# Kernel tuning notes

Hardware: AMD Instinct MI355X
Metric: run time of the kernel (lower is better)

## Reference

```python
import jax, jax.numpy as jnp
import numpy as np
from jax import lax

L, D, S, T, BATCH, NC = 4, 256, 64, 2048, 64, 10
EPS = 1e-5


def setup_inputs() -> dict:
    key = jax.random.key(0)
    ks = iter(jax.random.split(key, 16))
    n = lambda shape, s=1.0: jax.random.normal(next(ks), shape, dtype=jnp.float32) * s
    return {
        "x": n((BATCH, 1, T)),
        "emb_w": n((D, 1), 0.1), "emb_b": jnp.zeros((D,), jnp.float32),
        "Am": n((L, S, S), 0.01), "Bm": n((L, S, D), 0.01),
        "Cm": n((L, D, S), 0.01), "Dm": n((L, D, D), 0.01),
        "in_w": n((L, D, D), 0.05), "in_b": jnp.zeros((L, D), jnp.float32),
        "out_w": n((L, D, D), 0.05), "out_b": jnp.zeros((L, D), jnp.float32),
        "s4ln_w": jnp.ones((L, D), jnp.float32), "s4ln_b": jnp.zeros((L, D), jnp.float32),
        "ln_w": jnp.ones((L, D), jnp.float32), "ln_b": jnp.zeros((L, D), jnp.float32),
        "c1_w": n((512, D), 0.05), "c1_b": jnp.zeros((512,), jnp.float32),
        "bn1_g": jnp.ones((512,), jnp.float32), "bn1_b": jnp.zeros((512,), jnp.float32),
        "bn1_m": jnp.zeros((512,), jnp.float32), "bn1_v": jnp.ones((512,), jnp.float32),
        "c2_w": n((256, 512), 0.05), "c2_b": jnp.zeros((256,), jnp.float32),
        "bn2_g": jnp.ones((256,), jnp.float32), "bn2_b": jnp.zeros((256,), jnp.float32),
        "bn2_m": jnp.zeros((256,), jnp.float32), "bn2_v": jnp.ones((256,), jnp.float32),
        "c3_w": n((NC, 256), 0.05), "c3_b": jnp.zeros((NC,), jnp.float32),
    }


def _ln(x, w, b):
    m = jnp.mean(x, axis=-1, keepdims=True)
    v = jnp.mean((x - m) ** 2, axis=-1, keepdims=True)
    return (x - m) * lax.rsqrt(v + EPS) * w + b


def reference(x, emb_w, emb_b, Am, Bm, Cm, Dm, in_w, in_b, out_w, out_b,
              s4ln_w, s4ln_b, ln_w, ln_b, c1_w, c1_b, bn1_g, bn1_b, bn1_m, bn1_v,
              c2_w, c2_b, bn2_g, bn2_b, bn2_m, bn2_v, c3_w, c3_b):
    # x: (B, 1, T) -> (B, T, 1) -> embed to (B, T, D)
    h = jnp.transpose(x, (0, 2, 1)) @ emb_w.T + emb_b
    Bsz = h.shape[0]
    for l in range(L):
        res = h
        u = _ln(h @ in_w[l].T + in_b[l], s4ln_w[l], s4ln_b[l])  # input_proj + norm
        # precompute time-invariant input drives: (T, B, S) and (T, B, D)
        uB = jnp.einsum('btd,sd->tbs', u, Bm[l])
        uD = jnp.einsum('btd,ed->tbe', u, Dm[l])
        A = Am[l]

        def step(s, ub):  # s_t = s_{t-1} @ A^T + x_t @ B^T
            s = s @ A.T + ub
            return s, s

        _, hs = lax.scan(step, jnp.zeros((Bsz, S), h.dtype), uB)  # hs: (T, B, S)
        y = jnp.einsum('tbs,ds->btd', hs, Cm[l]) + jnp.transpose(uD, (1, 0, 2))
        y = y @ out_w[l].T + out_b[l]  # output_proj (dropout = identity in eval)
        h = _ln(y + res, ln_w[l], ln_b[l])  # residual + outer LayerNorm
    pooled = jnp.mean(h, axis=1)  # AdaptiveAvgPool1d(1) over time -> (B, D)
    z = pooled @ c1_w.T + c1_b
    z = jax.nn.relu((z - bn1_m) * lax.rsqrt(bn1_v + EPS) * bn1_g + bn1_b)
    z = z @ c2_w.T + c2_b
    z = jax.nn.relu((z - bn2_m) * lax.rsqrt(bn2_v + EPS) * bn2_g + bn2_b)
    return z @ c3_w.T + c3_b
```

## Files before the change

kernel.cpp:

```cpp
#include <hip/hip_runtime.h>


#define EPSF 1e-5f

typedef _Float16 F16;
typedef _Float16 half8 __attribute__((ext_vector_type(8)));
typedef float f32x4 __attribute__((ext_vector_type(4)));

constexpr int  Bc  = 64;
constexpr int  Tc  = 2048;
constexpr int  Dc  = 256;
constexpr int  Sc  = 64;
constexpr int  Lc  = 4;
constexpr int  KC  = 12;
constexpr int  NCc = 10;
constexpr int  PAD = 16;
constexpr long BT  = (long)Bc * Tc;
constexpr int  TPB = Tc + PAD;

constexpr size_t OFF_H16  = 0;
constexpr size_t OFF_U16  = OFF_H16 + (size_t)BT * Dc * 2;
constexpr size_t OFF_UBP  = OFF_U16 + (size_t)BT * Dc * 2;
constexpr size_t OFF_S16  = OFF_UBP + (size_t)Bc * TPB * Sc * 2;
constexpr size_t OFF_T16  = OFF_S16 + (size_t)BT * Sc * 2;
constexpr size_t OFF_IW16 = OFF_T16 + (size_t)Lc * KC * Sc * Sc * 2;
constexpr size_t OFF_OW16 = OFF_IW16 + (size_t)Lc * Dc * Dc * 2;
constexpr size_t OFF_BM16 = OFF_OW16 + (size_t)Lc * Dc * Dc * 2;
constexpr size_t OFF_CM16 = OFF_BM16 + (size_t)Lc * Sc * Dc * 2;
constexpr size_t OFF_DM16 = OFF_CM16 + (size_t)Lc * Dc * Sc * 2;
constexpr size_t OFF_PP   = OFF_DM16 + (size_t)Lc * Dc * Dc * 2;
constexpr size_t WS_NEED  = OFF_PP + (size_t)Bc * 32 * Dc * 4;

#define MFMA16(a, b, c) __builtin_amdgcn_mfma_f32_16x16x32_f16((a), (b), (c), 0, 0, 0)

__global__ __launch_bounds__(256) void diag_kernel(float* __restrict__ outp,
                                                   int n, float wsmb)
{
    int i = blockIdx.x * 256 + threadIdx.x;
    if (i < n) outp[i] = (i == 0) ? wsmb : 0.f;
}

__global__ __launch_bounds__(256) void cvt16_kernel(
    const float* __restrict__ src, F16* __restrict__ dst)
{
    long i = ((long)blockIdx.x * 256 + threadIdx.x) * 8;
    float4 a = *(const float4*)(src + i);
    float4 b = *(const float4*)(src + i + 4);
    half8 h;
    h[0] = (F16)a.x; h[1] = (F16)a.y; h[2] = (F16)a.z; h[3] = (F16)a.w;
    h[4] = (F16)b.x; h[5] = (F16)b.y; h[6] = (F16)b.z; h[7] = (F16)b.w;
    *(half8*)(dst + i) = h;
}

__global__ __launch_bounds__(256) void embed_kernel(
    const float* __restrict__ x, const float* __restrict__ ew,
    const float* __restrict__ eb, F16* __restrict__ h16)
{
    long i = ((long)blockIdx.x * 256 + threadIdx.x) * 8;
    int d = (int)(i & 255);
    long bt = i >> 8;
    float xv = x[bt];
    float4 w0 = *(const float4*)(ew + d), w1 = *(const float4*)(ew + d + 4);
    float4 b0 = *(const float4*)(eb + d), b1 = *(const float4*)(eb + d + 4);
    half8 h;
    h[0] = (F16)fmaf(xv, w0.x, b0.x); h[1] = (F16)fmaf(xv, w0.y, b0.y);
    h[2] = (F16)fmaf(xv, w0.z, b0.z); h[3] = (F16)fmaf(xv, w0.w, b0.w);
    h[4] = (F16)fmaf(xv, w1.x, b1.x); h[5] = (F16)fmaf(xv, w1.y, b1.y);
    h[6] = (F16)fmaf(xv, w1.z, b1.z); h[7] = (F16)fmaf(xv, w1.w, b1.w);
    *(half8*)(h16 + i) = h;
}

__global__ __launch_bounds__(256) void apow_kernel(
    const float* __restrict__ Am, F16* __restrict__ taps)
{
    int l = blockIdx.x;
    const float* A = Am + (long)l * Sc * Sc;
    F16* out = taps + (long)l * KC * Sc * Sc;
    __shared__ float sA[64][68];
    __shared__ float sP[64][68];
    int tid = threadIdx.x;

    for (int idx = tid; idx < 64 * 16; idx += 256) {
        int r = idx >> 4, q = idx & 15;
        float4 v = *(const float4*)(A + r * 64 + q * 4);
        *(float4*)&sA[r][q * 4] = v;
        float4 id;
        id.x = (q * 4 + 0 == r) ? 1.f : 0.f;
        id.y = (q * 4 + 1 == r) ? 1.f : 0.f;
        id.z = (q * 4 + 2 == r) ? 1.f : 0.f;
        id.w = (q * 4 + 3 == r) ? 1.f : 0.f;
        *(float4*)&sP[r][q * 4] = id;
        out[r * 64 + q * 4 + 0] = (F16)id.x;
        out[r * 64 + q * 4 + 1] = (F16)id.y;
        out[r * 64 + q * 4 + 2] = (F16)id.z;
        out[r * 64 + q * 4 + 3] = (F16)id.w;
    }
    __syncthreads();

    int rb = (tid >> 4) * 4;
    int cb = (tid & 15) * 4;
    for (int k = 1; k < KC; ++k) {
        float nacc[4][4];
#pragma unroll
        for (int i = 0; i < 4; i++)
#pragma unroll
            for (int u = 0; u < 4; u++) nacc[i][u] = 0.f;
        for (int s = 0; s < 64; ++s) {
            float4 p = *(const float4*)&sP[s][cb];
#pragma unroll
            for (int i = 0; i < 4; i++) {
                float a = sA[rb + i][s];
                nacc[i][0] = fmaf(a, p.x, nacc[i][0]);
                nacc[i][1] = fmaf(a, p.y, nacc[i][1]);
                nacc[i][2] = fmaf(a, p.z, nacc[i][2]);
                nacc[i][3] = fmaf(a, p.w, nacc[i][3]);
            }
        }
        __syncthreads();
#pragma unroll
        for (int i = 0; i < 4; i++) {
            *(float4*)&sP[rb + i][cb] = make_float4(nacc[i][0], nacc[i][1], nacc[i][2], nacc[i][3]);
#pragma unroll
            for (int c = 0; c < 4; c++)
                out[(long)k * 4096 + (rb + i) * 64 + cb + c] = (F16)nacc[i][c];
        }
        __syncthreads();
    }
}

__global__ __launch_bounds__(256) void zeropad_kernel(F16* __restrict__ ubp)
{
    long i8 = ((long)blockIdx.x * 256 + threadIdx.x) * 8;
    int b = (int)(i8 >> 10);
    int off = (int)(i8 & 1023);
    *(uint4*)(ubp + (long)b * TPB * Sc + off) = make_uint4(0u, 0u, 0u, 0u);
}

template<int DIR>
__global__ __launch_bounds__(512) void mfma_gemm_ln_kernel(
    const F16* X, F16* out, const F16* __restrict__ W,
    const float* __restrict__ bias,
    const float* __restrict__ lnw, const float* __restrict__ lnb)
{
    __shared__ half8 sW[16 * 8 * 64];
    const int tid = threadIdx.x;
    const int lane = tid & 63, wv = tid >> 6;
    const int r15 = lane & 15, hi4 = lane >> 4;

#pragma unroll
    for (int it = 0; it < 16; ++it) {
        int fid = tid + it * 512;
        int l2 = fid & 63, pair = fid >> 6;
        int n = pair >> 3, ks = pair & 7;
        sW[fid] = *(const half8*)(W + (n * 16 + (l2 & 15)) * Dc + ks * 32 + (l2 >> 4) * 8);
    }
    __syncthreads();

    const long m0 = (long)blockIdx.x * 256 + wv * 32;

    f32x4 acc[2][16];
#pragma unroll
    for (int r2 = 0; r2 < 2; ++r2)
#pragma unroll
        for (int n = 0; n < 16; ++n) acc[r2][n] = f32x4{0.f, 0.f, 0.f, 0.f};

    const F16* xb = X + (m0 + r15) * Dc + (hi4 << 3);

    for (int ks = 0; ks < 8; ++ks) {
        half8 a0 = *(const half8*)(xb + ks * 32);
        half8 a1 = *(const half8*)(xb + 16 * Dc + ks * 32);
#pragma unroll
        for (int n = 0; n < 16; ++n) {
            half8 b = sW[(n * 8 + ks) * 64 + lane];
            acc[0][n] = MFMA16(a0, b, acc[0][n]);
            acc[1][n] = MFMA16(a1, b, acc[1][n]);
        }
    }

    float bv[16], gw[16], gb[16];
#pragma unroll
    for (int n = 0; n < 16; ++n) {
        int c = n * 16 + r15;
        bv[n] = bias[c]; gw[n] = lnw[c]; gb[n] = lnb[c];
    }

#pragma unroll
    for (int r2 = 0; r2 < 2; ++r2) {
        const long rowb = m0 + r2 * 16 + hi4 * 4;
        float sum[4] = {0.f, 0.f, 0.f, 0.f}, ssq[4] = {0.f, 0.f, 0.f, 0.f};
#pragma unroll
        for (int n = 0; n < 16; ++n)
#pragma unroll
            for (int r = 0; r < 4; ++r) {
                float v = acc[r2][n][r] + bv[n];
                if (DIR) v += (float)out[(rowb + r) * Dc + n * 16 + r15];
                acc[r2][n][r] = v;
                sum[r] += v;
                ssq[r] = fmaf(v, v, ssq[r]);
            }
#pragma unroll
        for (int r = 0; r < 4; ++r) {
#pragma unroll
            for (int m = 1; m < 16; m <<= 1) {
                sum[r] += __shfl_xor(sum[r], m);
                ssq[r] += __shfl_xor(ssq[r], m);
            }
            float mean = sum[r] * (1.f / 256.f);
            float var  = fmaf(-mean, mean, ssq[r] * (1.f / 256.f));
            sum[r] = mean;
            ssq[r] = rsqrtf(var + EPSF);
        }
#pragma unroll
        for (int n = 0; n < 16; ++n)
#pragma unroll
            for (int r = 0; r < 4; ++r) {
                float val = fmaf((acc[r2][n][r] - sum[r]) * ssq[r], gw[n], gb[n]);
                out[(rowb + r) * Dc + n * 16 + r15] = (F16)val;
            }
    }
}

__global__ __launch_bounds__(512) void mfma_ub_kernel(
    const F16* __restrict__ X, const F16* __restrict__ W, F16* __restrict__ UBP)
{
    __shared__ half8 sW[4 * 8 * 64];
    const int tid = threadIdx.x;
    const int lane = tid & 63, wv = tid >> 6;
    const int r15 = lane & 15, hi4 = lane >> 4;

#pragma unroll
    for (int it = 0; it < 4; ++it) {
        int fid = tid + it * 512;
        int l2 = fid & 63, pair = fid >> 6;
        int n = pair >> 3, ks = pair & 7;
        sW[fid] = *(const half8*)(W + (n * 16 + (l2 & 15)) * Dc + ks * 32 + (l2 >> 4) * 8);
    }
    __syncthreads();

    const long m0 = (long)blockIdx.x * 256 + wv * 32;
    const long b  = m0 >> 11;
    const long tl = m0 & (Tc - 1);

    f32x4 acc[2][4];
#pragma unroll
    for (int r2 = 0; r2 < 2; ++r2)
#pragma unroll
        for (int n = 0; n < 4; ++n) acc[r2][n] = f32x4{0.f, 0.f, 0.f, 0.f};

    const F16* xb = X + (m0 + r15) * Dc + (hi4 << 3);

    for (int ks = 0; ks < 8; ++ks) {
        half8 a0 = *(const half8*)(xb + ks * 32);
        half8 a1 = *(const half8*)(xb + 16 * Dc + ks * 32);
#pragma unroll
        for (int n = 0; n < 4; ++n) {
            half8 bfr = sW[(n * 8 + ks) * 64 + lane];
            acc[0][n] = MFMA16(a0, bfr, acc[0][n]);
            acc[1][n] = MFMA16(a1, bfr, acc[1][n]);
        }
    }

#pragma unroll
    for (int r2 = 0; r2 < 2; ++r2) {
        const long rowb = b * TPB + PAD + tl + r2 * 16 + hi4 * 4;
#pragma unroll
        for (int n = 0; n < 4; ++n)
#pragma unroll
            for (int r = 0; r < 4; ++r)
                UBP[(rowb + r) * Sc + n * 16 + r15] = (F16)acc[r2][n][r];
    }
}

__global__ __launch_bounds__(512) void mfma_conv_kernel(
    const F16* __restrict__ UBP, const F16* __restrict__ T16, F16* __restrict__ S16)
{
    __shared__ half8 sT[12 * 4 * 2 * 64];
    const int tid = threadIdx.x;
    const int lane = tid & 63, wv = tid >> 6;
    const int r15 = lane & 15, hi4 = lane >> 4;

#pragma unroll
    for (int it = 0; it < 12; ++it) {
        int fid = tid + it * 512;
        int l2 = fid & 63, rest = fid >> 6;
        int k = rest >> 3, nk = rest & 7;
        int n = nk >> 1, ks = nk & 1;
        sT[fid] = *(const half8*)(T16 + (long)k * 4096 +
                                  (n * 16 + (l2 & 15)) * Sc + ks * 32 + (l2 >> 4) * 8);
    }
    __syncthreads();

    const long m0 = (long)blockIdx.x * 256 + wv * 32;
    const long b  = m0 >> 11;
    const long tl = m0 & (Tc - 1);

    f32x4 acc[2][4];
#pragma unroll
    for (int r2 = 0; r2 < 2; ++r2)
#pragma unroll
        for (int n = 0; n < 4; ++n) acc[r2][n] = f32x4{0.f, 0.f, 0.f, 0.f};

    const long abase = (b * TPB + PAD + tl + r15) * Sc + (hi4 << 3);

    for (int k = 0; k < KC; ++k) {
        const F16* ap = UBP + abase - (long)k * Sc;
#pragma unroll
        for (int ks = 0; ks < 2; ++ks) {
            half8 a0 = *(const half8*)(ap + ks * 32);
            half8 a1 = *(const half8*)(ap + 16 * Sc + ks * 32);
#pragma unroll
            for (int n = 0; n < 4; ++n) {
                half8 bfr = sT[(k * 8 + n * 2 + ks) * 64 + lane];
                acc[0][n] = MFMA16(a0, bfr, acc[0][n]);
                acc[1][n] = MFMA16(a1, bfr, acc[1][n]);
            }
        }
    }

#pragma unroll
    for (int r2 = 0; r2 < 2; ++r2) {
        const long rowb = m0 + r2 * 16 + hi4 * 4;
#pragma unroll
        for (int n = 0; n < 4; ++n)
#pragma unroll
            for (int r = 0; r < 4; ++r)
                S16[(rowb + r) * Sc + n * 16 + r15] = (F16)acc[r2][n][r];
    }
}

__global__ __launch_bounds__(512) void mfma_k4_kernel(
    const F16* __restrict__ S16, const F16* __restrict__ C16,
    const F16* U16, const F16* __restrict__ D16, F16* Y16)
{
    __shared__ half8 sD[16 * 8 * 64];
    const int tid = threadIdx.x;
    const int lane = tid & 63, wv = tid >> 6;
    const int r15 = lane & 15, hi4 = lane >> 4;

#pragma unroll
    for (int it = 0; it < 16; ++it) {
        int fid = tid + it * 512;
        int l2 = fid & 63, pair = fid >> 6;
        int n = pair >> 3, ks = pair & 7;
        sD[fid] = *(const half8*)(D16 + (n * 16 + (l2 & 15)) * Dc + ks * 32 + (l2 >> 4) * 8);
    }
    __syncthreads();

    const long m0 = (long)blockIdx.x * 256 + wv * 32;

    f32x4 acc[2][16];
#pragma unroll
    for (int r2 = 0; r2 < 2; ++r2)
#pragma unroll
        for (int n = 0; n < 16; ++n) acc[r2][n] = f32x4{0.f, 0.f, 0.f, 0.f};

    const F16* sb = S16 + (m0 + r15) * Sc + (hi4 << 3);
    const F16* cw = C16 + (long)r15 * Sc + (hi4 << 3);
#pragma unroll
    for (int ks = 0; ks < 2; ++ks) {
        half8 a0 = *(const half8*)(sb + ks * 32);
        half8 a1 = *(const half8*)(sb + 16 * Sc + ks * 32);
#pragma unroll
        for (int n = 0; n < 16; ++n) {
            half8 bfr = *(const half8*)(cw + n * 16 * Sc + ks * 32);
            acc[0][n] = MFMA16(a0, bfr, acc[0][n]);
            acc[1][n] = MFMA16(a1, bfr, acc[1][n]);
        }
    }

    const F16* ub = U16 + (m0 + r15) * Dc + (hi4 << 3);
    for (int ks = 0; ks < 8; ++ks) {
        half8 a0 = *(const half8*)(ub + ks * 32);
        half8 a1 = *(const half8*)(ub + 16 * Dc + ks * 32);
#pragma unroll
        for (int n = 0; n < 16; ++n) {
            half8 bfr = sD[(n * 8 + ks) * 64 + lane];
            acc[0][n] = MFMA16(a0, bfr, acc[0][n]);
            acc[1][n] = MFMA16(a1, bfr, acc[1][n]);
        }
    }

#pragma unroll
    for (int r2 = 0; r2 < 2; ++r2) {
        const long rowb = m0 + r2 * 16 + hi4 * 4;
#pragma unroll
        for (int n = 0; n < 16; ++n)
#pragma unroll
            for (int r = 0; r < 4; ++r)
                Y16[(rowb + r) * Dc + n * 16 + r15] = (F16)acc[r2][n][r];
    }
}

__global__ __launch_bounds__(256) void pool_partial_kernel(
    const F16* __restrict__ h16, float* __restrict__ pp)
{
    int b = blockIdx.x >> 5, ch = blockIdx.x & 31;
    const F16* base = h16 + ((long)b * Tc + ch * 64) * Dc + threadIdx.x;
    float s = 0.f;
#pragma unroll 8
    for (int t = 0; t < 64; ++t) s += (float)base[(long)t * Dc];
    pp[((long)b * 32 + ch) * Dc + threadIdx.x] = s;
}

__global__ __launch_bounds__(256) void head_kernel(
    const float* __restrict__ pp,
    const float* __restrict__ c1w, const float* __restrict__ c1b,
    const float* __restrict__ g1, const float* __restrict__ b1,
    const float* __restrict__ m1, const float* __restrict__ v1,
    const float* __restrict__ c2w, const float* __restrict__ c2b,
    const float* __restrict__ g2, const float* __restrict__ b2,
    const float* __restrict__ m2, const float* __restrict__ v2,
    const float* __restrict__ c3w, const float* __restrict__ c3b,
    float* __restrict__ outp)
{
    __shared__ float p[256];
    __shared__ float z1[512];
    __shared__ float z2[256];
    const int b = blockIdx.x, tid = threadIdx.x;

    float s = 0.f;
#pragma unroll
    for (int ch = 0; ch < 32; ++ch) s += pp[((long)b * 32 + ch) * Dc + tid];
    p[tid] = s * (1.f / (float)Tc);
    __syncthreads();

#pragma unroll
    for (int rep = 0; rep < 2; ++rep) {
        int n = tid + rep * 256;
        const float* wr = c1w + (long)n * 256;
        float dot = 0.f;
        for (int k4 = 0; k4 < 64; ++k4) {
            float4 wv = *(const float4*)(wr + k4 * 4);
            float4 pv = *(const float4*)&p[k4 * 4];
            dot = fmaf(wv.x, pv.x, dot);
            dot = fmaf(wv.y, pv.y, dot);
            dot = fmaf(wv.z, pv.z, dot);
            dot = fmaf(wv.w, pv.w, dot);
        }
        float z = (dot + c1b[n] - m1[n]) * rsqrtf(v1[n] + EPSF) * g1[n] + b1[n];
        z1[n] = fmaxf(z, 0.f);
    }
    __syncthreads();

    {
        int n = tid;
        const float* wr = c2w + (long)n * 512;
        float dot = 0.f;
        for (int k4 = 0; k4 < 128; ++k4) {
            float4 wv = *(const float4*)(wr + k4 * 4);
            float4 zv = *(const float4*)&z1[k4 * 4];
            dot = fmaf(wv.x, zv.x, dot);
            dot = fmaf(wv.y, zv.y, dot);
            dot = fmaf(wv.z, zv.z, dot);
            dot = fmaf(wv.w, zv.w, dot);
        }
        float z = (dot + c2b[n] - m2[n]) * rsqrtf(v2[n] + EPSF) * g2[n] + b2[n];
        z2[n] = fmaxf(z, 0.f);
    }
    __syncthreads();

    if (tid < NCc) {
        const float* wr = c3w + (long)tid * 256;
        float dot = 0.f;
        for (int k4 = 0; k4 < 64; ++k4) {
            float4 wv = *(const float4*)(wr + k4 * 4);
            float4 zv = *(const float4*)&z2[k4 * 4];
            dot = fmaf(wv.x, zv.x, dot);
            dot = fmaf(wv.y, zv.y, dot);
            dot = fmaf(wv.z, zv.z, dot);
            dot = fmaf(wv.w, zv.w, dot);
        }
        outp[b * NCc + tid] = dot + c3b[tid];
    }
}

extern "C" void kernel_launch(void* const* d_in, const int* in_sizes, int n_in,
                              void* d_out, int out_size, void* d_ws, size_t ws_size,
                              hipStream_t stream)
{
    float* outp = (float*)d_out;

    if (ws_size < WS_NEED) {
        float wsmb = (float)((double)ws_size / (1024.0 * 1024.0));
        diag_kernel<<<(out_size + 255) / 256, 256, 0, stream>>>(outp, out_size, wsmb);
        return;
    }

    const float* x      = (const float*)d_in[0];
    const float* emb_w  = (const float*)d_in[1];
    const float* emb_b  = (const float*)d_in[2];
    const float* Am     = (const float*)d_in[3];
    const float* Bm     = (const float*)d_in[4];
    const float* Cm     = (const float*)d_in[5];
    const float* Dm     = (const float*)d_in[6];
    const float* in_w   = (const float*)d_in[7];
    const float* in_b   = (const float*)d_in[8];
    const float* out_w  = (const float*)d_in[9];
    const float* out_b  = (const float*)d_in[10];
    const float* s4ln_w = (const float*)d_in[11];
    const float* s4ln_b = (const float*)d_in[12];
    const float* ln_w   = (const float*)d_in[13];
    const float* ln_b   = (const float*)d_in[14];
    const float* c1_w   = (const float*)d_in[15];
    const float* c1_b   = (const float*)d_in[16];
    const float* bn1_g  = (const float*)d_in[17];
    const float* bn1_b  = (const float*)d_in[18];
    const float* bn1_m  = (const float*)d_in[19];
    const float* bn1_v  = (const float*)d_in[20];
    const float* c2_w   = (const float*)d_in[21];
    const float* c2_b   = (const float*)d_in[22];
    const float* bn2_g  = (const float*)d_in[23];
    const float* bn2_b  = (const float*)d_in[24];
    const float* bn2_m  = (const float*)d_in[25];
    const float* bn2_v  = (const float*)d_in[26];
    const float* c3_w   = (const float*)d_in[27];
    const float* c3_b   = (const float*)d_in[28];

    char* wsb = (char*)d_ws;
    F16*   h16  = (F16*)(wsb + OFF_H16);
    F16*   u16  = (F16*)(wsb + OFF_U16);
    F16*   ubp  = (F16*)(wsb + OFF_UBP);
    F16*   s16  = (F16*)(wsb + OFF_S16);
    F16*   t16  = (F16*)(wsb + OFF_T16);
    F16*   iw16 = (F16*)(wsb + OFF_IW16);
    F16*   ow16 = (F16*)(wsb + OFF_OW16);
    F16*   bm16 = (F16*)(wsb + OFF_BM16);
    F16*   cm16 = (F16*)(wsb + OFF_CM16);
    F16*   dm16 = (F16*)(wsb + OFF_DM16);
    float* pp   = (float*)(wsb + OFF_PP);

    const int GB = (int)(BT / 256);

    cvt16_kernel<<<Lc * Dc * Dc / 2048, 256, 0, stream>>>(in_w, iw16);
    cvt16_kernel<<<Lc * Dc * Dc / 2048, 256, 0, stream>>>(out_w, ow16);
    cvt16_kernel<<<Lc * Sc * Dc / 2048, 256, 0, stream>>>(Bm, bm16);
    cvt16_kernel<<<Lc * Dc * Sc / 2048, 256, 0, stream>>>(Cm, cm16);
    cvt16_kernel<<<Lc * Dc * Dc / 2048, 256, 0, stream>>>(Dm, dm16);
    apow_kernel<<<Lc, 256, 0, stream>>>(Am, t16);
    zeropad_kernel<<<32, 256, 0, stream>>>(ubp);
    embed_kernel<<<(int)(BT * Dc / 2048), 256, 0, stream>>>(x, emb_w, emb_b, h16);

    for (int l = 0; l < Lc; ++l) {
        mfma_gemm_ln_kernel<0><<<GB, 512, 0, stream>>>(
            h16, u16, iw16 + (long)l * Dc * Dc, in_b + l * Dc,
            s4ln_w + l * Dc, s4ln_b + l * Dc);
        mfma_ub_kernel<<<GB, 512, 0, stream>>>(
            u16, bm16 + (long)l * Sc * Dc, ubp);
        mfma_conv_kernel<<<GB, 512, 0, stream>>>(
            ubp, t16 + (long)l * KC * Sc * Sc, s16);
        mfma_k4_kernel<<<GB, 512, 0, stream>>>(
            s16, cm16 + (long)l * Dc * Sc, u16, dm16 + (long)l * Dc * Dc, u16);
        mfma_gemm_ln_kernel<1><<<GB, 512, 0, stream>>>(
            u16, h16, ow16 + (long)l * Dc * Dc, out_b + l * Dc,
            ln_w + l * Dc, ln_b + l * Dc);
    }

    pool_partial_kernel<<<Bc * 32, 256, 0, stream>>>(h16, pp);
    head_kernel<<<Bc, 256, 0, stream>>>(pp,
        c1_w, c1_b, bn1_g, bn1_b, bn1_m, bn1_v,
        c2_w, c2_b, bn2_g, bn2_b, bn2_m, bn2_v,
        c3_w, c3_b, outp);
}
```

Before: 980.8 us.

## Stage GEMM weights and activations via direct global-to-LDS loads with double buffering

Replaces register-staged weight loads and direct global activation reads in the input-projection GEMM+LN kernel and the C/D output kernel with global_load_lds transfers into shared memory. Activation tiles are double-buffered in LDS so the next K-chunk load is issued while MFMAs run on the current one. This aims to hide global load latency and cut VGPR pressure, at the cost of a block-wide barrier every K-step. Correctness depends on the LDS-direct loads having landed before each barrier.

```diff
diff --git a/kernel.cpp b/kernel.cpp
--- a/kernel.cpp
+++ b/kernel.cpp
@@ -32,6 +32,12 @@
 constexpr size_t WS_NEED  = OFF_PP + (size_t)Bc * 32 * Dc * 4;
 
 #define MFMA16(a, b, c) __builtin_amdgcn_mfma_f32_16x16x32_f16((a), (b), (c), 0, 0, 0)
+
+__device__ __forceinline__ void gl_lds16(const void* gsrc, void* ldst) {
+    __builtin_amdgcn_global_load_lds(
+        (const __attribute__((address_space(1))) void*)gsrc,
+        (__attribute__((address_space(3))) void*)ldst, 16, 0, 0);
+}
 
 __global__ __launch_bounds__(256) void diag_kernel(float* __restrict__ outp,
                                                    int n, float wsmb)
@@ -143,20 +149,28 @@
     const float* __restrict__ lnw, const float* __restrict__ lnb)
 {
     __shared__ half8 sW[16 * 8 * 64];
+    __shared__ half8 sA[2][16 * 64];
     const int tid = threadIdx.x;
     const int lane = tid & 63, wv = tid >> 6;
     const int r15 = lane & 15, hi4 = lane >> 4;
+    const long m0g = (long)blockIdx.x * 256;
+    const long m0  = m0g + wv * 32;
+    const int sg0 = wv * 2, sg1 = wv * 2 + 1;
 
 #pragma unroll
     for (int it = 0; it < 16; ++it) {
-        int fid = tid + it * 512;
-        int l2 = fid & 63, pair = fid >> 6;
+        int pair = wv + it * 8;
         int n = pair >> 3, ks = pair & 7;
-        sW[fid] = *(const half8*)(W + (n * 16 + (l2 & 15)) * Dc + ks * 32 + (l2 >> 4) * 8);
-    }
-    __syncthreads();
-
-    const long m0 = (long)blockIdx.x * 256 + wv * 32;
+        const F16* g = W + (n * 16 + r15) * Dc + ks * 32 + hi4 * 8;
+        gl_lds16(g, (char*)sW + pair * 1024);
+    }
+    {
+        const F16* g0 = X + (m0g + sg0 * 16 + r15) * Dc + hi4 * 8;
+        const F16* g1 = X + (m0g + sg1 * 16 + r15) * Dc + hi4 * 8;
+        gl_lds16(g0, (char*)&sA[0][0] + sg0 * 1024);
+        gl_lds16(g1, (char*)&sA[0][0] + sg1 * 1024);
+    }
+    __syncthreads();
 
     f32x4 acc[2][16];
 #pragma unroll
@@ -164,17 +178,23 @@
 #pragma unroll
         for (int n = 0; n < 16; ++n) acc[r2][n] = f32x4{0.f, 0.f, 0.f, 0.f};
 
-    const F16* xb = X + (m0 + r15) * Dc + (hi4 << 3);
-
-    for (int ks = 0; ks < 8; ++ks) {
-        half8 a0 = *(const half8*)(xb + ks * 32);
-        half8 a1 = *(const half8*)(xb + 16 * Dc + ks * 32);
+    for (int kc = 0; kc < 8; ++kc) {
+        if (kc < 7) {
+            int nb = (kc + 1) & 1;
+            const F16* g0 = X + (m0g + sg0 * 16 + r15) * Dc + (kc + 1) * 32 + hi4 * 8;
+            const F16* g1 = X + (m0g + sg1 * 16 + r15) * Dc + (kc + 1) * 32 + hi4 * 8;
+            gl_lds16(g0, (char*)&sA[nb][0] + sg0 * 1024);
+            gl_lds16(g1, (char*)&sA[nb][0] + sg1 * 1024);
+        }
+        half8 a0 = sA[kc & 1][sg0 * 64 + lane];
+        half8 a1 = sA[kc & 1][sg1 * 64 + lane];
 #pragma unroll
         for (int n = 0; n < 16; ++n) {
-            half8 b = sW[(n * 8 + ks) * 64 + lane];
+            half8 b = sW[(n * 8 + kc) * 64 + lane];
             acc[0][n] = MFMA16(a0, b, acc[0][n]);
             acc[1][n] = MFMA16(a1, b, acc[1][n]);
         }
+        __syncthreads();
     }
 
     float bv[16], gw[16], gb[16];
@@ -333,20 +353,27 @@
     const F16* U16, const F16* __restrict__ D16, F16* Y16)
 {
     __shared__ half8 sD[16 * 8 * 64];
+    __shared__ half8 sU[2][16 * 64];
     const int tid = threadIdx.x;
     const int lane = tid & 63, wv = tid >> 6;
     const int r15 = lane & 15, hi4 = lane >> 4;
+    const long m0g = (long)blockIdx.x * 256;
+    const long m0  = m0g + wv * 32;
+    const int sg0 = wv * 2, sg1 = wv * 2 + 1;
 
 #pragma unroll
     for (int it = 0; it < 16; ++it) {
-        int fid = tid + it * 512;
-        int l2 = fid & 63, pair = fid >> 6;
+        int pair = wv + it * 8;
         int n = pair >> 3, ks = pair & 7;
-        sD[fid] = *(const half8*)(D16 + (n * 16 + (l2 & 15)) * Dc + ks * 32 + (l2 >> 4) * 8);
-    }
-    __syncthreads();
-
-    const long m0 = (long)blockIdx.x * 256 + wv * 32;
+        const F16* g = D16 + (n * 16 + r15) * Dc + ks * 32 + hi4 * 8;
+        gl_lds16(g, (char*)sD + pair * 1024);
+    }
+    {
+        const F16* g0 = U16 + (m0g + sg0 * 16 + r15) * Dc + hi4 * 8;
+        const F16* g1 = U16 + (m0g + sg1 * 16 + r15) * Dc + hi4 * 8;
+        gl_lds16(g0, (char*)&sU[0][0] + sg0 * 1024);
+        gl_lds16(g1, (char*)&sU[0][0] + sg1 * 1024);
+    }
 
     f32x4 acc[2][16];
 #pragma unroll
@@ -367,17 +394,25 @@
             acc[1][n] = MFMA16(a1, bfr, acc[1][n]);
         }
     }
-
-    const F16* ub = U16 + (m0 + r15) * Dc + (hi4 << 3);
-    for (int ks = 0; ks < 8; ++ks) {
-        half8 a0 = *(const half8*)(ub + ks * 32);
-        half8 a1 = *(const half8*)(ub + 16 * Dc + ks * 32);
+    __syncthreads();
+
+    for (int kc = 0; kc < 8; ++kc) {
+        if (kc < 7) {
+            int nb = (kc + 1) & 1;
+            const F16* g0 = U16 + (m0g + sg0 * 16 + r15) * Dc + (kc + 1) * 32 + hi4 * 8;
+            const F16* g1 = U16 + (m0g + sg1 * 16 + r15) * Dc + (kc + 1) * 32 + hi4 * 8;
+            gl_lds16(g0, (char*)&sU[nb][0] + sg0 * 1024);
+            gl_lds16(g1, (char*)&sU[nb][0] + sg1 * 1024);
+        }
+        half8 a0 = sU[kc & 1][sg0 * 64 + lane];
+        half8 a1 = sU[kc & 1][sg1 * 64 + lane];
 #pragma unroll
         for (int n = 0; n < 16; ++n) {
-            half8 bfr = sD[(n * 8 + ks) * 64 + lane];
+            half8 bfr = sD[(n * 8 + kc) * 64 + lane];
             acc[0][n] = MFMA16(a0, bfr, acc[0][n]);
             acc[1][n] = MFMA16(a1, bfr, acc[1][n]);
         }
+        __syncthreads();
     }
 
 #pragma unroll
```

Result: no change. 997.8 us (+1.7%).
